# Kernel tuning notes

Hardware: AMD Instinct MI355X
Metric: run time of the kernel (lower is better)

Reference implementation:

```python
import jax, jax.numpy as jnp
import numpy as np

GRID_SIZE = 5
SPLINE_ORDER = 3
N_COEF = GRID_SIZE + SPLINE_ORDER  # 8
NUM_NODES = 100000
NUM_EDGES = 1200000
NUM_GRAPHS = 512
D = 64
N_TARGETS = 10


def _grid():
    # uniform grid on [-1, 1] extended by spline_order knots on each side (efficient-kan default)
    h = 2.0 / GRID_SIZE
    return jnp.arange(-SPLINE_ORDER, GRID_SIZE + SPLINE_ORDER + 1, dtype=jnp.float32) * h - 1.0


def b_splines(x):
    # x: (N, in) -> (N, in, N_COEF) via Cox-de Boor recursion
    g = _grid()
    xe = x[..., None]
    bases = ((xe >= g[:-1]) & (xe < g[1:])).astype(x.dtype)
    for k in range(1, SPLINE_ORDER + 1):
        left = (xe - g[: -(k + 1)]) / (g[k:-1] - g[: -(k + 1)])
        right = (g[k + 1:] - xe) / (g[k + 1:] - g[1:-k])
        bases = left * bases[..., :-1] + right * bases[..., 1:]
    return bases


def kan_linear(x, base_w, spline_w, scaler):
    # efficient-kan KANLinear: silu base branch + standalone-scaled spline branch
    base = jax.nn.silu(x) @ base_w.T
    sb = b_splines(x)  # (N, in, N_COEF)
    spline = jnp.einsum('nig,oig->no', sb, spline_w * scaler[..., None])
    return base + spline


def setup_inputs() -> dict:
    key = jax.random.key(0)
    ks = jax.random.split(key, 12)
    inp = {
        'x': jax.random.normal(ks[0], (NUM_NODES, D), dtype=jnp.float32),
        'edge_index': jax.random.randint(ks[1], (2, NUM_EDGES), 0, NUM_NODES, dtype=jnp.int64),
        'batch': jnp.sort(jax.random.randint(ks[2], (NUM_NODES,), 0, NUM_GRAPHS, dtype=jnp.int64)),
        # GINConv layer 0 KAN (D -> D)
        'base_w0': jax.random.normal(ks[3], (D, D), dtype=jnp.float32) * 0.1,
        'spline_w0': jax.random.normal(ks[4], (D, D, N_COEF), dtype=jnp.float32) * 0.1,
        'scaler0': jax.random.normal(ks[5], (D, D), dtype=jnp.float32) * 0.1 + 1.0,
        # GINConv layer 1 KAN (D -> D)
        'base_w1': jax.random.normal(ks[6], (D, D), dtype=jnp.float32) * 0.1,
        'spline_w1': jax.random.normal(ks[7], (D, D, N_COEF), dtype=jnp.float32) * 0.1,
        'scaler1': jax.random.normal(ks[8], (D, D), dtype=jnp.float32) * 0.1 + 1.0,
        # head KAN (D -> N_TARGETS)
        'base_wh': jax.random.normal(ks[9], (N_TARGETS, D), dtype=jnp.float32) * 0.1,
        'spline_wh': jax.random.normal(ks[10], (N_TARGETS, D, N_COEF), dtype=jnp.float32) * 0.1,
        'scaler_h': jax.random.normal(ks[11], (N_TARGETS, D), dtype=jnp.float32) * 0.1 + 1.0,
    }
    return inp


def reference(x, edge_index, batch, base_w0, spline_w0, scaler0,
              base_w1, spline_w1, scaler1, base_wh, spline_wh, scaler_h):
    src, dst = edge_index[0], edge_index[1]
    n = x.shape[0]
    # GINConv layer 0: nn((1+eps)*x + sum_{j in N(i)} x_j), eps=0; dropout is eval-mode identity
    agg = jax.ops.segment_sum(x[src], dst, num_segments=n)
    h = kan_linear(x + agg, base_w0, spline_w0, scaler0)
    # GINConv layer 1
    agg = jax.ops.segment_sum(h[src], dst, num_segments=n)
    h = kan_linear(h + agg, base_w1, spline_w1, scaler1)
    # global_add_pool over graphs, then KAN head
    pooled = jax.ops.segment_sum(h, batch, num_segments=NUM_GRAPHS)
    return kan_linear(pooled, base_wh, spline_wh, scaler_h)
```

## Files before the change

kernel.cpp:

```cpp
#include <hip/hip_runtime.h>
#include <hip/hip_fp16.h>
#include <math.h>

#define NODES   100000
#define EDGES   1200000
#define GRAPHS  512
#define DIM     64
#define NT      10
#define KTOT    576

#define NB      512
#define NBUSED  391
#define EPB     4096
#define CAP     4608

#define KSTAGE     64
#define WTL_STRIDE 72
#define V_STRIDE   72

#define S3B     ((EDGES + EPB - 1) / EPB)
#define PREPB   ((2 * DIM * KTOT) / 512)
#define CONVB   ((NODES * 16 + 32 + 511) / 512)

typedef _Float16 f16x8  __attribute__((ext_vector_type(8)));
typedef __fp16   fp16x2 __attribute__((ext_vector_type(2)));
typedef __attribute__((ext_vector_type(4))) float frag_cd;

__device__ __forceinline__ float silu(float x) {
    return x * __builtin_amdgcn_rcpf(1.f + __expf(-x));
}

__device__ __forceinline__ unsigned packh2(float a, float b) {
    fp16x2 h = __builtin_amdgcn_cvt_pkrtz(a, b);
    return __builtin_bit_cast(unsigned, h);
}

union H8 { uint4 u; __half2 h[4]; };

__device__ __forceinline__ f16x8 bases_frag(float xv) {
    float tt  = fmaf(xv, 2.5f, 5.5f);
    float fm  = floorf(tt);
    int   m   = (int)fm;
    float u   = tt - fm;
    float u2  = u * u;
    float u3  = u2 * u;
    float v0  = fmaf(fmaf(fmaf(u, -(1.f / 6.f), 0.5f), u, -0.5f), u, 1.f / 6.f);
    float v1  = fmaf(u3, 0.5f, fmaf(u2, -1.f, 2.f / 3.f));
    float v2  = fmaf(u + u2 - u3, 0.5f, 1.f / 6.f);
    float v3  = u3 * (1.f / 6.f);

    unsigned d0 = packh2(v0, v1);
    unsigned d1 = packh2(v2, v3);
    int p = m - 3;
    int B = p >> 1;
    bool odd = (p & 1) != 0;
    unsigned e1 = __builtin_amdgcn_alignbit(d1, d0, 16);
    unsigned W0 = odd ? (d0 << 16) : d0;
    unsigned W1 = odd ? e1 : d1;
    unsigned W2 = odd ? (d1 >> 16) : 0u;
    union { f16x8 f; unsigned u[4]; } r;
    r.u[0] = (B == 0) ? W0 : ((B == -1) ? W1 : ((B == -2) ? W2 : 0u));
    r.u[1] = (B == 1) ? W0 : ((B ==  0) ? W1 : ((B == -1) ? W2 : 0u));
    r.u[2] = (B == 2) ? W0 : ((B ==  1) ? W1 : ((B ==  0) ? W2 : 0u));
    r.u[3] = (B == 3) ? W0 : ((B ==  2) ? W1 : ((B ==  1) ? W2 : 0u));
    return r.f;
}

__global__ __launch_bounds__(512) void mega(const int* __restrict__ ei,
                                            int* __restrict__ bcur,
                                            unsigned* __restrict__ tmp,
                                            const float* __restrict__ bw0,
                                            const float* __restrict__ sw0,
                                            const float* __restrict__ sc0,
                                            const float* __restrict__ bw1,
                                            const float* __restrict__ sw1,
                                            const float* __restrict__ sc1,
                                            unsigned short* __restrict__ wt0,
                                            unsigned short* __restrict__ wt1,
                                            const float* __restrict__ x,
                                            const int* __restrict__ bat,
                                            unsigned short* __restrict__ xb,
                                            unsigned short* __restrict__ hpad,
                                            int* __restrict__ goff) {
    __shared__ int hist[NB], lstart[NB], gbase[NB], cur[NB];
    __shared__ unsigned ebuf[EPB];
    __shared__ unsigned short bk[EPB];
    const int bx = blockIdx.x;
    const int t  = threadIdx.x;

    if (bx < S3B) {
        hist[t] = 0; cur[t] = 0;
        __syncthreads();
        const int e0 = bx * EPB;
        int src[8], dst[8];
#pragma unroll
        for (int k = 0; k < 8; ++k) {
            int e = e0 + t + k * 512;
            bool valid = e < EDGES;
            src[k] = valid ? ei[e] : 0;
            dst[k] = valid ? ei[EDGES + e] : -1;
            if (valid) atomicAdd(&hist[dst[k] >> 8], 1);
        }
        __syncthreads();
        int v = hist[t];
        lstart[t] = v;
        __syncthreads();
        int run = v;
        for (int d = 1; d < NB; d <<= 1) {
            int a = (t >= d) ? lstart[t - d] : 0;
            __syncthreads();
            run += a; lstart[t] = run;
            __syncthreads();
        }
        lstart[t] = run - v;
        if (v) gbase[t] = atomicAdd(&bcur[t], v);
        __syncthreads();
#pragma unroll
        for (int k = 0; k < 8; ++k) {
            if (dst[k] >= 0) {
                int b = dst[k] >> 8;
                int pos = lstart[b] + atomicAdd(&cur[b], 1);
                ebuf[pos] = (unsigned)src[k] | ((unsigned)(dst[k] & 255) << 24);
                bk[pos] = (unsigned short)b;
            }
        }
        __syncthreads();
        int total = EDGES - e0; if (total > EPB) total = EPB;
        for (int i = t; i < total; i += 512) {
            int b = bk[i];
            tmp[(size_t)b * CAP + gbase[b] + (i - lstart[b])] = ebuf[i];
        }
        return;
    }

    if (bx < S3B + PREPB) {
        int idx = (bx - S3B) * 512 + t;
        int layer = idx >= DIM * KTOT;
        int li = layer ? idx - DIM * KTOT : idx;
        const float* bw = layer ? bw1 : bw0;
        const float* sw = layer ? sw1 : sw0;
        const float* sc = layer ? sc1 : sc0;
        unsigned short* wt = layer ? wt1 : wt0;
        int o = li / KTOT, k = li % KTOT;
        float v;
        if (k < DIM) {
            v = bw[o * DIM + k];
        } else {
            int i = (k - DIM) >> 3, g = (k - DIM) & 7;
            v = sw[(o * DIM + i) * 8 + g] * sc[o * DIM + i];
        }
        wt[li] = __half_as_ushort(__float2half(v));
        return;
    }

    int i = (bx - S3B - PREPB) * 512 + t;
    if (i < NODES * 16) {
        float4 v = ((const float4*)x)[i];
        unsigned lo = packh2(v.x, v.y);
        unsigned hi = packh2(v.z, v.w);
        ((uint2*)xb)[i] = make_uint2(lo, hi);
        if ((i & 15) == 0) {
            int n = i >> 4;
            int b  = bat[n];
            int bp = (n == 0) ? -1 : bat[n - 1];
            for (int g = bp + 1; g <= b; ++g) goff[g] = n;
        }
        if (i == 0) {
            int blast = bat[NODES - 1];
            for (int g = blast + 1; g <= GRAPHS; ++g) goff[g] = NODES;
        }
    } else {
        int j = i - NODES * 16;
        if (j < 16)      ((uint2*)xb)[NODES * 16 + j] = make_uint2(0, 0);
        else if (j < 32) ((uint2*)hpad)[j - 16]       = make_uint2(0, 0);
    }
}

__global__ __launch_bounds__(1024) void s4_fill(const unsigned* __restrict__ tmp,
                                                const int* __restrict__ bcur,
                                                int2* __restrict__ rowp,
                                                int* __restrict__ col) {
    __shared__ int deg[256], scanI[256], cur[256];
    __shared__ int tot;
    __shared__ int4 colbuf4[CAP / 4];
    int* colbuf = (int*)colbuf4;
    const int b = blockIdx.x, t = threadIdx.x;
    const int cnt = bcur[b];
    const int base = b * CAP;
    if (t < 256) deg[t] = 0;
    __syncthreads();
    for (int i = t; i < cnt; i += 1024)
        atomicAdd(&deg[tmp[base + i] >> 24], 1);
    __syncthreads();
    if (t < 256) scanI[t] = (deg[t] + 3) & ~3;
    __syncthreads();
    for (int d = 1; d < 256; d <<= 1) {
        int a = 0;
        if (t < 256 && t >= d) a = scanI[t - d];
        __syncthreads();
        if (t < 256) scanI[t] += a;
        __syncthreads();
    }
    if (t < 256) {
        int pad = (deg[t] + 3) & ~3;
        int start = scanI[t] - pad;
        int ng = b * 256 + t;
        if (ng < NODES) rowp[ng] = make_int2(base + start, base + start + pad);
        cur[t] = start;
        if (t == 255) tot = scanI[255];
    }
    __syncthreads();
    for (int i = t; i < cnt; i += 1024) {
        unsigned p = tmp[base + i];
        int pos = atomicAdd(&cur[p >> 24], 1);
        colbuf[pos] = (int)(p & 0xFFFFFFu);
    }
    __syncthreads();
    if (t < 256) {
        int pad = (deg[t] + 3) & ~3;
        int end = scanI[t] - pad + pad;
        for (int k = cur[t]; k < end; ++k) colbuf[k] = NODES;
    }
    __syncthreads();
    int nq = tot >> 2;
    int4* out4 = (int4*)(col + base);
    for (int i = t; i < nq; i += 1024) out4[i] = colbuf4[i];
}

__global__ __launch_bounds__(256, 8) void fused_layer(const unsigned short* __restrict__ xin,
                                                      const int2* __restrict__ rowp,
                                                      const int* __restrict__ col,
                                                      const unsigned short* __restrict__ wt,
                                                      unsigned short* __restrict__ out) {
    __shared__ unsigned short wt_lds[64 * WTL_STRIDE];
    __shared__ unsigned short v_lds[64 * V_STRIDE];

    const int t     = threadIdx.x;
    const int nbase = blockIdx.x * 64;

    uint4 p0, p1;
    {
        int c0 = t, c1 = t + 256;
        p0 = *(const uint4*)(wt + (c0 >> 3) * KTOT + (c0 & 7) * 8);
        p1 = *(const uint4*)(wt + (c1 >> 3) * KTOT + (c1 & 7) * 8);
    }

    const uint4* x4 = (const uint4*)xin;
#pragma unroll
    for (int rd = 0; rd < 2; ++rd) {
        int idx  = t + rd * 256;
        int node = idx >> 3, c8 = idx & 7;
        int n = nbase + node;
        uint4 res = make_uint4(0, 0, 0, 0);
        if (n < NODES) {
            int2 be = rowp[n];
            H8 a0, a1, a2, a3;
            a0.u = x4[n * 8 + c8];
            a1.u = make_uint4(0, 0, 0, 0);
            a2.u = make_uint4(0, 0, 0, 0);
            a3.u = make_uint4(0, 0, 0, 0);
            for (int p = be.x; p < be.y; p += 4) {
                int4 c4 = *(const int4*)(col + p);
                H8 r0, r1, r2, r3;
                r0.u = x4[c4.x * 8 + c8];
                r1.u = x4[c4.y * 8 + c8];
                r2.u = x4[c4.z * 8 + c8];
                r3.u = x4[c4.w * 8 + c8];
#pragma unroll
                for (int j = 0; j < 4; ++j) {
                    a0.h[j] = __hadd2(a0.h[j], r0.h[j]);
                    a1.h[j] = __hadd2(a1.h[j], r1.h[j]);
                    a2.h[j] = __hadd2(a2.h[j], r2.h[j]);
                    a3.h[j] = __hadd2(a3.h[j], r3.h[j]);
                }
            }
#pragma unroll
            for (int j = 0; j < 4; ++j)
                a0.h[j] = __hadd2(__hadd2(a0.h[j], a1.h[j]), __hadd2(a2.h[j], a3.h[j]));
            res = a0.u;
        }
        *(uint4*)(v_lds + node * V_STRIDE + c8 * 8) = res;
    }
    {
        int c0 = t, c1 = t + 256;
        *(uint4*)(wt_lds + (c0 >> 3) * WTL_STRIDE + (c0 & 7) * 8) = p0;
        *(uint4*)(wt_lds + (c1 >> 3) * WTL_STRIDE + (c1 & 7) * 8) = p1;
    }
    __syncthreads();

    const int w = t >> 6;
    const int l = t & 63;
    const int q = l >> 4;
    const int c = l & 15;
    const unsigned short* vrow = v_lds + ((w << 4) + c) * V_STRIDE;

    frag_cd ac0 = {0.f, 0.f, 0.f, 0.f};
    frag_cd ac1 = {0.f, 0.f, 0.f, 0.f};
    frag_cd ac2 = {0.f, 0.f, 0.f, 0.f};
    frag_cd ac3 = {0.f, 0.f, 0.f, 0.f};

#define MSTEP(OFF, A) {                                                          \
        f16x8 b0 = *(const f16x8*)(wt_lds + (c     ) * WTL_STRIDE + (OFF));      \
        f16x8 b1 = *(const f16x8*)(wt_lds + (c + 16) * WTL_STRIDE + (OFF));      \
        f16x8 b2 = *(const f16x8*)(wt_lds + (c + 32) * WTL_STRIDE + (OFF));      \
        f16x8 b3 = *(const f16x8*)(wt_lds + (c + 48) * WTL_STRIDE + (OFF));      \
        ac0 = __builtin_amdgcn_mfma_f32_16x16x32_f16(A, b0, ac0, 0, 0, 0);       \
        ac1 = __builtin_amdgcn_mfma_f32_16x16x32_f16(A, b1, ac1, 0, 0, 0);       \
        ac2 = __builtin_amdgcn_mfma_f32_16x16x32_f16(A, b2, ac2, 0, 0, 0);       \
        ac3 = __builtin_amdgcn_mfma_f32_16x16x32_f16(A, b3, ac3, 0, 0, 0); }

    {
        int c0 = t, c1 = t + 256;
        p0 = *(const uint4*)(wt + (c0 >> 3) * KTOT + KSTAGE + (c0 & 7) * 8);
        p1 = *(const uint4*)(wt + (c1 >> 3) * KTOT + KSTAGE + (c1 & 7) * 8);
    }

#pragma unroll
    for (int s = 0; s < 2; ++s) {
        f16x8 hv = *(const f16x8*)(vrow + 32 * s + 8 * q);
        float f[8];
#pragma unroll
        for (int j = 0; j < 8; ++j) f[j] = silu((float)hv[j]);
        union { f16x8 v; unsigned u[4]; } a;
#pragma unroll
        for (int j = 0; j < 4; ++j) a.u[j] = packh2(f[2 * j], f[2 * j + 1]);
        MSTEP(32 * s + 8 * q, a.v);
    }

#pragma unroll
    for (int st = 1; st < 9; ++st) {
        __syncthreads();
        {
            int c0 = t, c1 = t + 256;
            *(uint4*)(wt_lds + (c0 >> 3) * WTL_STRIDE + (c0 & 7) * 8) = p0;
            *(uint4*)(wt_lds + (c1 >> 3) * WTL_STRIDE + (c1 & 7) * 8) = p1;
        }
        __syncthreads();
        if (st < 8) {
            int c0 = t, c1 = t + 256;
            p0 = *(const uint4*)(wt + (c0 >> 3) * KTOT + (st + 1) * KSTAGE + (c0 & 7) * 8);
            p1 = *(const uint4*)(wt + (c1 >> 3) * KTOT + (st + 1) * KSTAGE + (c1 & 7) * 8);
        }
#pragma unroll
        for (int k2 = 0; k2 < 2; ++k2) {
            f16x8 a = bases_frag((float)(*(const _Float16*)(vrow + 8 * (st - 1) + 4 * k2 + q)));
            MSTEP(32 * k2 + 8 * q, a);
        }
    }
#undef MSTEP

    const int n0 = nbase + (w << 4) + (q << 2);
#pragma unroll
    for (int r = 0; r < 4; ++r) {
        int n = n0 + r;
        if (n < NODES) {
            unsigned short* o = out + (size_t)n * DIM + c;
            o[0]  = __half_as_ushort(__float2half(ac0[r]));
            o[16] = __half_as_ushort(__float2half(ac1[r]));
            o[32] = __half_as_ushort(__float2half(ac2[r]));
            o[48] = __half_as_ushort(__float2half(ac3[r]));
        }
    }
}

__global__ __launch_bounds__(256) void pool_head(const unsigned short* __restrict__ h,
                                                 const int* __restrict__ goff,
                                                 const float* __restrict__ bwh,
                                                 const float* __restrict__ swh,
                                                 const float* __restrict__ sch,
                                                 float* __restrict__ out) {
    __shared__ float ps[8][64];
    const int g = blockIdx.x, t = threadIdx.x;
    const int start = goff[g], end = goff[g + 1];
    const int d2 = t & 31, grp = t >> 5;
    float s0 = 0.f, s1 = 0.f;
    for (int n = start + grp; n < end; n += 8) {
        __half2 hv = *(const __half2*)(h + (size_t)n * DIM + 2 * d2);
        float2 f = __half22float2(hv);
        s0 += f.x;
        s1 += f.y;
    }
    ps[grp][2 * d2]     = s0;
    ps[grp][2 * d2 + 1] = s1;
    __syncthreads();

    if (t < 64) {
        const int i = t;
        float xv = 0.f;
#pragma unroll
        for (int k = 0; k < 8; ++k) xv += ps[k][i];

        float s  = silu(xv);
        float tt  = fmaf(xv, 2.5f, 5.5f);
        float fm  = floorf(tt);
        int   m   = (int)fm;
        float u   = tt - fm;
        float u2  = u * u;
        float u3  = u2 * u;
        float v0  = fmaf(fmaf(fmaf(u, -(1.f / 6.f), 0.5f), u, -0.5f), u, 1.f / 6.f);
        float v1  = fmaf(u3, 0.5f, fmaf(u2, -1.f, 2.f / 3.f));
        float v2  = fmaf(u + u2 - u3, 0.5f, 1.f / 6.f);
        float v3  = u3 * (1.f / 6.f);
        bool inr  = (m >= 0) && (m <= 10);
        float b[8];
#pragma unroll
        for (int j = 0; j < 8; ++j) {
            float bv = 0.f;
            bv = (j == m - 3) ? v0 : bv;
            bv = (j == m - 2) ? v1 : bv;
            bv = (j == m - 1) ? v2 : bv;
            bv = (j == m)     ? v3 : bv;
            b[j] = inr ? bv : 0.f;
        }

        float part[NT];
#pragma unroll
        for (int o = 0; o < NT; ++o) {
            const float* sp = swh + (o * DIM + i) * 8;
            float sb = 0.f;
#pragma unroll
            for (int qq = 0; qq < 8; ++qq) sb = fmaf(b[qq], sp[qq], sb);
            part[o] = fmaf(s, bwh[o * DIM + i], sb * sch[o * DIM + i]);
        }
#pragma unroll
        for (int o = 0; o < NT; ++o) {
            float v = part[o];
#pragma unroll
            for (int off = 32; off > 0; off >>= 1) v += __shfl_down(v, off, 64);
            if (i == 0) out[g * NT + o] = v;
        }
    }
}

extern "C" void kernel_launch(void* const* d_in, const int* in_sizes, int n_in,
                              void* d_out, int out_size, void* d_ws, size_t ws_size,
                              hipStream_t stream) {
    const float* x   = (const float*)d_in[0];
    const int*   ei  = (const int*)d_in[1];
    const int*   bat = (const int*)d_in[2];
    const float* bw0 = (const float*)d_in[3];
    const float* sw0 = (const float*)d_in[4];
    const float* sc0 = (const float*)d_in[5];
    const float* bw1 = (const float*)d_in[6];
    const float* sw1 = (const float*)d_in[7];
    const float* sc1 = (const float*)d_in[8];
    const float* bwh = (const float*)d_in[9];
    const float* swh = (const float*)d_in[10];
    const float* sch = (const float*)d_in[11];
    float* out = (float*)d_out;

    const size_t ROW = (size_t)(NODES + 1) * DIM;

    unsigned short* wt0 = (unsigned short*)d_ws;
    unsigned short* wt1 = wt0 + DIM * KTOT;
    unsigned short* xbf = wt1 + DIM * KTOT;
    unsigned short* hbf = xbf + ROW;
    unsigned short* h2  = hbf + ROW;
    int* goff     = (int*)(h2 + (size_t)NODES * DIM);
    int2* rowp    = (int2*)(goff + 514);
    int* col      = (int*)(rowp + NODES);
    int* bcur     = col + (size_t)NB * CAP;
    unsigned* tmp = (unsigned*)(bcur + NB);

    (void)hipMemsetAsync(bcur, 0, NB * sizeof(int), stream);

    mega<<<S3B + PREPB + CONVB, 512, 0, stream>>>(
        ei, bcur, tmp,
        bw0, sw0, sc0, bw1, sw1, sc1, wt0, wt1,
        x, bat, xbf, hbf + (size_t)NODES * DIM, goff);

    s4_fill<<<NBUSED, 1024, 0, stream>>>(tmp, bcur, rowp, col);

    const int layer_blocks = (NODES + 63) / 64;
    fused_layer<<<layer_blocks, 256, 0, stream>>>(xbf, rowp, col, wt0, hbf);
    fused_layer<<<layer_blocks, 256, 0, stream>>>(hbf, rowp, col, wt1, h2);

    pool_head<<<GRAPHS, 256, 0, stream>>>(h2, goff, bwh, swh, sch, out);
}
```

Before: 200.9 us.

## Fuse global add-pool into second GIN layer via atomics, prefetch neighbor indices

The second fused layer now accumulates its outputs directly into a per-graph fp32 pooled buffer with atomicAdd. When four consecutive nodes share a graph they are pre-summed into one atomic, which removes the h2 write and the separate pool pass; the head becomes a tiny 64-thread kernel. The gather loop prefetches the next column-index quad and uses two accumulators instead of four, and s4_fill writes a 4-entry sentinel pad so the prefetch past the row end stays valid. This trades a global store plus reread for atomic contention on 512x64 floats. Pooling order also becomes nondeterministic.

After: 209.7 us. 4.4% more time.

```diff
diff --git a/kernel.cpp b/kernel.cpp
--- a/kernel.cpp
+++ b/kernel.cpp
@@ -78,10 +78,8 @@
                                             unsigned short* __restrict__ wt0,
                                             unsigned short* __restrict__ wt1,
                                             const float* __restrict__ x,
-                                            const int* __restrict__ bat,
                                             unsigned short* __restrict__ xb,
-                                            unsigned short* __restrict__ hpad,
-                                            int* __restrict__ goff) {
+                                            unsigned short* __restrict__ hpad) {
     __shared__ int hist[NB], lstart[NB], gbase[NB], cur[NB];
     __shared__ unsigned ebuf[EPB];
     __shared__ unsigned short bk[EPB];
@@ -159,16 +157,6 @@
         unsigned lo = packh2(v.x, v.y);
         unsigned hi = packh2(v.z, v.w);
         ((uint2*)xb)[i] = make_uint2(lo, hi);
-        if ((i & 15) == 0) {
-            int n = i >> 4;
-            int b  = bat[n];
-            int bp = (n == 0) ? -1 : bat[n - 1];
-            for (int g = bp + 1; g <= b; ++g) goff[g] = n;
-        }
-        if (i == 0) {
-            int blast = bat[NODES - 1];
-            for (int g = blast + 1; g <= GRAPHS; ++g) goff[g] = NODES;
-        }
     } else {
         int j = i - NODES * 16;
         if (j < 16)      ((uint2*)xb)[NODES * 16 + j] = make_uint2(0, 0);
@@ -225,13 +213,17 @@
     int nq = tot >> 2;
     int4* out4 = (int4*)(col + base);
     for (int i = t; i < nq; i += 1024) out4[i] = colbuf4[i];
-}
-
+    if (t < 4) col[base + tot + t] = NODES;
+}
+
+template<int POOL>
 __global__ __launch_bounds__(256, 8) void fused_layer(const unsigned short* __restrict__ xin,
                                                       const int2* __restrict__ rowp,
                                                       const int* __restrict__ col,
                                                       const unsigned short* __restrict__ wt,
-                                                      unsigned short* __restrict__ out) {
+                                                      unsigned short* __restrict__ out,
+                                                      const int* __restrict__ bat,
+                                                      float* __restrict__ pooled) {
     __shared__ unsigned short wt_lds[64 * WTL_STRIDE];
     __shared__ unsigned short v_lds[64 * V_STRIDE];
 
@@ -254,13 +246,12 @@
         uint4 res = make_uint4(0, 0, 0, 0);
         if (n < NODES) {
             int2 be = rowp[n];
-            H8 a0, a1, a2, a3;
+            H8 a0, a1;
             a0.u = x4[n * 8 + c8];
             a1.u = make_uint4(0, 0, 0, 0);
-            a2.u = make_uint4(0, 0, 0, 0);
-            a3.u = make_uint4(0, 0, 0, 0);
+            int4 c4 = *(const int4*)(col + be.x);
             for (int p = be.x; p < be.y; p += 4) {
-                int4 c4 = *(const int4*)(col + p);
+                int4 c4n = *(const int4*)(col + p + 4);
                 H8 r0, r1, r2, r3;
                 r0.u = x4[c4.x * 8 + c8];
                 r1.u = x4[c4.y * 8 + c8];
@@ -268,15 +259,13 @@
                 r3.u = x4[c4.w * 8 + c8];
 #pragma unroll
                 for (int j = 0; j < 4; ++j) {
-                    a0.h[j] = __hadd2(a0.h[j], r0.h[j]);
-                    a1.h[j] = __hadd2(a1.h[j], r1.h[j]);
-                    a2.h[j] = __hadd2(a2.h[j], r2.h[j]);
-                    a3.h[j] = __hadd2(a3.h[j], r3.h[j]);
+                    a0.h[j] = __hadd2(a0.h[j], __hadd2(r0.h[j], r1.h[j]));
+                    a1.h[j] = __hadd2(a1.h[j], __hadd2(r2.h[j], r3.h[j]));
                 }
+                c4 = c4n;
             }
 #pragma unroll
-            for (int j = 0; j < 4; ++j)
-                a0.h[j] = __hadd2(__hadd2(a0.h[j], a1.h[j]), __hadd2(a2.h[j], a3.h[j]));
+            for (int j = 0; j < 4; ++j) a0.h[j] = __hadd2(a0.h[j], a1.h[j]);
             res = a0.u;
         }
         *(uint4*)(v_lds + node * V_STRIDE + c8 * 8) = res;
@@ -350,85 +339,91 @@
 #undef MSTEP
 
     const int n0 = nbase + (w << 4) + (q << 2);
-#pragma unroll
-    for (int r = 0; r < 4; ++r) {
-        int n = n0 + r;
-        if (n < NODES) {
-            unsigned short* o = out + (size_t)n * DIM + c;
-            o[0]  = __half_as_ushort(__float2half(ac0[r]));
-            o[16] = __half_as_ushort(__float2half(ac1[r]));
-            o[32] = __half_as_ushort(__float2half(ac2[r]));
-            o[48] = __half_as_ushort(__float2half(ac3[r]));
-        }
-    }
-}
-
-__global__ __launch_bounds__(256) void pool_head(const unsigned short* __restrict__ h,
-                                                 const int* __restrict__ goff,
-                                                 const float* __restrict__ bwh,
-                                                 const float* __restrict__ swh,
-                                                 const float* __restrict__ sch,
-                                                 float* __restrict__ out) {
-    __shared__ float ps[8][64];
-    const int g = blockIdx.x, t = threadIdx.x;
-    const int start = goff[g], end = goff[g + 1];
-    const int d2 = t & 31, grp = t >> 5;
-    float s0 = 0.f, s1 = 0.f;
-    for (int n = start + grp; n < end; n += 8) {
-        __half2 hv = *(const __half2*)(h + (size_t)n * DIM + 2 * d2);
-        float2 f = __half22float2(hv);
-        s0 += f.x;
-        s1 += f.y;
-    }
-    ps[grp][2 * d2]     = s0;
-    ps[grp][2 * d2 + 1] = s1;
-    __syncthreads();
-
-    if (t < 64) {
-        const int i = t;
-        float xv = 0.f;
-#pragma unroll
-        for (int k = 0; k < 8; ++k) xv += ps[k][i];
-
-        float s  = silu(xv);
-        float tt  = fmaf(xv, 2.5f, 5.5f);
-        float fm  = floorf(tt);
-        int   m   = (int)fm;
-        float u   = tt - fm;
-        float u2  = u * u;
-        float u3  = u2 * u;
-        float v0  = fmaf(fmaf(fmaf(u, -(1.f / 6.f), 0.5f), u, -0.5f), u, 1.f / 6.f);
-        float v1  = fmaf(u3, 0.5f, fmaf(u2, -1.f, 2.f / 3.f));
-        float v2  = fmaf(u + u2 - u3, 0.5f, 1.f / 6.f);
-        float v3  = u3 * (1.f / 6.f);
-        bool inr  = (m >= 0) && (m <= 10);
-        float b[8];
-#pragma unroll
-        for (int j = 0; j < 8; ++j) {
-            float bv = 0.f;
-            bv = (j == m - 3) ? v0 : bv;
-            bv = (j == m - 2) ? v1 : bv;
-            bv = (j == m - 1) ? v2 : bv;
-            bv = (j == m)     ? v3 : bv;
-            b[j] = inr ? bv : 0.f;
-        }
-
-        float part[NT];
-#pragma unroll
-        for (int o = 0; o < NT; ++o) {
-            const float* sp = swh + (o * DIM + i) * 8;
-            float sb = 0.f;
-#pragma unroll
-            for (int qq = 0; qq < 8; ++qq) sb = fmaf(b[qq], sp[qq], sb);
-            part[o] = fmaf(s, bwh[o * DIM + i], sb * sch[o * DIM + i]);
-        }
-#pragma unroll
-        for (int o = 0; o < NT; ++o) {
-            float v = part[o];
-#pragma unroll
-            for (int off = 32; off > 0; off >>= 1) v += __shfl_down(v, off, 64);
-            if (i == 0) out[g * NT + o] = v;
-        }
+    if (POOL == 0) {
+#pragma unroll
+        for (int r = 0; r < 4; ++r) {
+            int n = n0 + r;
+            if (n < NODES) {
+                unsigned short* o = out + (size_t)n * DIM + c;
+                o[0]  = __half_as_ushort(__float2half(ac0[r]));
+                o[16] = __half_as_ushort(__float2half(ac1[r]));
+                o[32] = __half_as_ushort(__float2half(ac2[r]));
+                o[48] = __half_as_ushort(__float2half(ac3[r]));
+            }
+        }
+    } else {
+        bool full = (n0 + 3 < NODES);
+        int g0 = full ? bat[n0] : 0;
+        int g3 = full ? bat[n0 + 3] : -1;
+        if (full && g0 == g3) {
+            float* pp = pooled + g0 * DIM + c;
+            atomicAdd(pp,      ac0[0] + ac0[1] + ac0[2] + ac0[3]);
+            atomicAdd(pp + 16, ac1[0] + ac1[1] + ac1[2] + ac1[3]);
+            atomicAdd(pp + 32, ac2[0] + ac2[1] + ac2[2] + ac2[3]);
+            atomicAdd(pp + 48, ac3[0] + ac3[1] + ac3[2] + ac3[3]);
+        } else {
+#pragma unroll
+            for (int r = 0; r < 4; ++r) {
+                int n = n0 + r;
+                if (n < NODES) {
+                    int g = bat[n];
+                    float* pp = pooled + g * DIM + c;
+                    atomicAdd(pp,      ac0[r]);
+                    atomicAdd(pp + 16, ac1[r]);
+                    atomicAdd(pp + 32, ac2[r]);
+                    atomicAdd(pp + 48, ac3[r]);
+                }
+            }
+        }
+    }
+}
+
+__global__ __launch_bounds__(64) void head_k(const float* __restrict__ pooled,
+                                             const float* __restrict__ bwh,
+                                             const float* __restrict__ swh,
+                                             const float* __restrict__ sch,
+                                             float* __restrict__ out) {
+    const int g = blockIdx.x, i = threadIdx.x;
+    float xv = pooled[g * DIM + i];
+
+    float s  = silu(xv);
+    float tt  = fmaf(xv, 2.5f, 5.5f);
+    float fm  = floorf(tt);
+    int   m   = (int)fm;
+    float u   = tt - fm;
+    float u2  = u * u;
+    float u3  = u2 * u;
+    float v0  = fmaf(fmaf(fmaf(u, -(1.f / 6.f), 0.5f), u, -0.5f), u, 1.f / 6.f);
+    float v1  = fmaf(u3, 0.5f, fmaf(u2, -1.f, 2.f / 3.f));
+    float v2  = fmaf(u + u2 - u3, 0.5f, 1.f / 6.f);
+    float v3  = u3 * (1.f / 6.f);
+    bool inr  = (m >= 0) && (m <= 10);
+    float b[8];
+#pragma unroll
+    for (int j = 0; j < 8; ++j) {
+        float bv = 0.f;
+        bv = (j == m - 3) ? v0 : bv;
+        bv = (j == m - 2) ? v1 : bv;
+        bv = (j == m - 1) ? v2 : bv;
+        bv = (j == m)     ? v3 : bv;
+        b[j] = inr ? bv : 0.f;
+    }
+
+    float part[NT];
+#pragma unroll
+    for (int o = 0; o < NT; ++o) {
+        const float* sp = swh + (o * DIM + i) * 8;
+        float sb = 0.f;
+#pragma unroll
+        for (int qq = 0; qq < 8; ++qq) sb = fmaf(b[qq], sp[qq], sb);
+        part[o] = fmaf(s, bwh[o * DIM + i], sb * sch[o * DIM + i]);
+    }
+#pragma unroll
+    for (int o = 0; o < NT; ++o) {
+        float v = part[o];
+#pragma unroll
+        for (int off = 32; off > 0; off >>= 1) v += __shfl_down(v, off, 64);
+        if (i == 0) out[g * NT + o] = v;
     }
 }
 
@@ -455,25 +450,24 @@
     unsigned short* wt1 = wt0 + DIM * KTOT;
     unsigned short* xbf = wt1 + DIM * KTOT;
     unsigned short* hbf = xbf + ROW;
-    unsigned short* h2  = hbf + ROW;
-    int* goff     = (int*)(h2 + (size_t)NODES * DIM);
-    int2* rowp    = (int2*)(goff + 514);
+    int2* rowp    = (int2*)(hbf + ROW);
     int* col      = (int*)(rowp + NODES);
     int* bcur     = col + (size_t)NB * CAP;
-    unsigned* tmp = (unsigned*)(bcur + NB);
-
-    (void)hipMemsetAsync(bcur, 0, NB * sizeof(int), stream);
+    float* pooled = (float*)(bcur + NB);
+    unsigned* tmp = (unsigned*)(pooled + (size_t)GRAPHS * DIM);
+
+    (void)hipMemsetAsync(bcur, 0, NB * sizeof(int) + (size_t)GRAPHS * DIM * sizeof(float), stream);
 
     mega<<<S3B + PREPB + CONVB, 512, 0, stream>>>(
         ei, bcur, tmp,
         bw0, sw0, sc0, bw1, sw1, sc1, wt0, wt1,
-        x, bat, xbf, hbf + (size_t)NODES * DIM, goff);
+        x, xbf, hbf + (size_t)NODES * DIM);
 
     s4_fill<<<NBUSED, 1024, 0, stream>>>(tmp, bcur, rowp, col);
 
     const int layer_blocks = (NODES + 63) / 64;
-    fused_layer<<<layer_blocks, 256, 0, stream>>>(xbf, rowp, col, wt0, hbf);
-    fused_layer<<<layer_blocks, 256, 0, stream>>>(hbf, rowp, col, wt1, h2);
-
-    pool_head<<<GRAPHS, 256, 0, stream>>>(h2, goff, bwh, swh, sch, out);
-}
+    fused_layer<0><<<layer_blocks, 256, 0, stream>>>(xbf, rowp, col, wt0, hbf, nullptr, nullptr);
+    fused_layer<1><<<layer_blocks, 256, 0, stream>>>(hbf, rowp, col, wt1, nullptr, bat, pooled);
+
+    head_k<<<GRAPHS, 64, 0, stream>>>(pooled, bwh, swh, sch, out);
+}
```
